# Kernel optimization log

Measured on AMD Instinct MI355X. Metric: run time of the kernel, lower is better.

The kernel has to match this reference:

```python
import jax, jax.numpy as jnp
import numpy as np


def setup_inputs() -> dict:
    key = jax.random.key(0)
    ks = jax.random.split(key, 7)
    b, c, t, h, w = 2, 64, 8, 32, 32
    d = 64
    return {
        "video_features": jax.random.normal(ks[0], (b, c, t, h, w), dtype=jnp.float32),
        "wq": jax.random.normal(ks[1], (d, c), dtype=jnp.float32) * 0.05,
        "bq": jax.random.normal(ks[2], (d,), dtype=jnp.float32) * 0.05,
        "wk": jax.random.normal(ks[3], (d, c), dtype=jnp.float32) * 0.05,
        "bk": jax.random.normal(ks[4], (d,), dtype=jnp.float32) * 0.05,
        "wv": jax.random.normal(ks[5], (d, c), dtype=jnp.float32) * 0.05,
        "bv": jax.random.normal(ks[6], (d,), dtype=jnp.float32) * 0.05,
    }


def reference(video_features, wq, bq, wk, bk, wv, bv):
    b, c, t, h, w = video_features.shape
    d = wq.shape[0]
    xf = video_features.reshape(b, c, t * h * w)  # [b, c, N]
    # 1x1x1 Conv3d == channel-wise linear projection
    q = jnp.einsum('dc,bcn->bnd', wq, xf) + bq                 # [b, N, d]
    k = jnp.einsum('dc,bcn->bnd', wk, xf) + bk                 # [b, N, d]
    v = jnp.einsum('dc,bcn->bnd', wv, xf) + bv                 # [b, N, d]
    scores = jnp.einsum('bnd,bmd->bnm', q, k) / jnp.sqrt(jnp.asarray(d, xf.dtype))  # [b, N, N]
    attn = jax.nn.softmax(scores, axis=-1)
    out = jnp.einsum('bnm,bmd->bnd', attn, v)                  # [b, N, d]
    out = out.transpose(0, 2, 1).reshape(b, d, t, h, w)
    out = out.sum(axis=2).reshape(b, d, 1, h, w)
    return out
```

## Files before the change

kernel.cpp:

```cpp
#include <hip/hip_runtime.h>
#include <math.h>

#define B 2
#define D 64
#define N 8192
#define T 8
#define HW 1024
#define NCH 8
#define KPC (N / NCH)
#define KT 64
#define NT (KPC / KT)
#define QT 256
#define NQT (N / QT)
#define PTS 18

#define LOG2E 1.44269504f

typedef _Float16 half8 __attribute__((ext_vector_type(8)));
typedef _Float16 half4 __attribute__((ext_vector_type(4)));
typedef _Float16 half2 __attribute__((ext_vector_type(2)));
typedef float floatx4 __attribute__((ext_vector_type(4)));

__global__ __launch_bounds__(256)
void proj_kernel(const float* __restrict__ x,
                 const float* __restrict__ wq, const float* __restrict__ bq,
                 const float* __restrict__ wk, const float* __restrict__ bk,
                 const float* __restrict__ wv, const float* __restrict__ bv,
                 _Float16* __restrict__ Qh, _Float16* __restrict__ Kh,
                 _Float16* __restrict__ VTh) {
    int n  = blockIdx.x * 256 + threadIdx.x;
    int d0 = blockIdx.y * 4;
    int b  = blockIdx.z;

    float xcol[64];
    const float* xb = x + (size_t)b * 64 * N + n;
#pragma unroll
    for (int c = 0; c < 64; ++c) xcol[c] = xb[(size_t)c * N];

    float aq[4], ak[4], av[4];
#pragma unroll
    for (int i = 0; i < 4; ++i) { aq[i] = bq[d0+i]; ak[i] = bk[d0+i]; av[i] = bv[d0+i]; }
#pragma unroll
    for (int c = 0; c < 64; ++c) {
        float xv = xcol[c];
#pragma unroll
        for (int i = 0; i < 4; ++i) {
            aq[i] += wq[(d0 + i) * 64 + c] * xv;
            ak[i] += wk[(d0 + i) * 64 + c] * xv;
            av[i] += wv[(d0 + i) * 64 + c] * xv;
        }
    }
    size_t rowb = ((size_t)b * N + n) * 64 + d0;
    half4 hq, hk;
    const float qs = 0.125f * LOG2E;
#pragma unroll
    for (int i = 0; i < 4; ++i) {
        hq[i] = (_Float16)(aq[i] * qs);
        hk[i] = (_Float16)ak[i];
    }
    *(half4*)(Qh + rowb) = hq;
    *(half4*)(Kh + rowb) = hk;
#pragma unroll
    for (int i = 0; i < 4; ++i)
        VTh[((size_t)b * 64 + d0 + i) * N + n] = (_Float16)av[i];
}

__global__ __launch_bounds__(256, 2)
void attn_kernel(const _Float16* __restrict__ Qh, const _Float16* __restrict__ Kh,
                 const _Float16* __restrict__ VTh,
                 _Float16* __restrict__ Opart, float* __restrict__ lpart) {
    __shared__ _Float16 Ks[2][64][72];
    __shared__ _Float16 VTs[2][64][72];

    int bid = blockIdx.x;
    int b   = bid / (NCH * NQT);
    int rem = bid % (NCH * NQT);
    int ch  = rem / NQT;
    int qt  = rem % NQT;
    int q0  = qt * QT;
    int kbase = ch * KPC;

    int tid  = threadIdx.x;
    int wave = tid >> 6;
    int lane = tid & 63;
    int L    = lane & 15;
    int quad = lane >> 4;

    half8 qa[4][2];
#pragma unroll
    for (int g = 0; g < 4; ++g) {
        const _Float16* qrow = Qh + ((size_t)b * N + q0 + wave * 64 + g * 16 + L) * 64;
        qa[g][0] = *(const half8*)(qrow + quad * 8);
        qa[g][1] = *(const half8*)(qrow + 32 + quad * 8);
    }

    floatx4 o[4][4];
    floatx4 lacc[4];
#pragma unroll
    for (int g = 0; g < 4; ++g) {
        lacc[g] = (floatx4)0.f;
#pragma unroll
        for (int s = 0; s < 4; ++s) o[g][s] = (floatx4)0.f;
    }

    half8 ones;
    {
        _Float16 v = (L == 0) ? (_Float16)1.0f : (_Float16)0.0f;
#pragma unroll
        for (int i = 0; i < 8; ++i) ones[i] = v;
    }

    int srow = tid >> 2, sseg = tid & 3;
    const _Float16* Kg = Kh  + (size_t)b * N * 64 + (size_t)sseg * 16;
    const _Float16* Vg = VTh + ((size_t)b * 64 + srow) * N + sseg * 16;

    half8 kr0, kr1, vr0, vr1;
    {
        const _Float16* kp = Kg + (size_t)(kbase + srow) * 64;
        kr0 = *(const half8*)(kp);
        kr1 = *(const half8*)(kp + 8);
        const _Float16* vp = Vg + kbase;
        vr0 = *(const half8*)(vp);
        vr1 = *(const half8*)(vp + 8);
    }
    *(half8*)(&Ks[0][srow][sseg * 16])      = kr0;
    *(half8*)(&Ks[0][srow][sseg * 16 + 8])  = kr1;
    *(half8*)(&VTs[0][srow][sseg * 16])     = vr0;
    *(half8*)(&VTs[0][srow][sseg * 16 + 8]) = vr1;
    __syncthreads();

    for (int kt = 0; kt < NT; ++kt) {
        int cur = kt & 1, nxt = cur ^ 1;
        bool more = (kt + 1 < NT);

        if (more) {
            int kb = kbase + (kt + 1) * KT;
            const _Float16* kp = Kg + (size_t)(kb + srow) * 64;
            kr0 = *(const half8*)(kp);
            kr1 = *(const half8*)(kp + 8);
            const _Float16* vp = Vg + kb;
            vr0 = *(const half8*)(vp);
            vr1 = *(const half8*)(vp + 8);
        }

        half8 kf[4][2], vb[4][2];
#pragma unroll
        for (int sub = 0; sub < 4; ++sub) {
            kf[sub][0] = *(const half8*)(&Ks[cur][sub * 16 + L][quad * 8]);
            kf[sub][1] = *(const half8*)(&Ks[cur][sub * 16 + L][32 + quad * 8]);
            vb[sub][0] = *(const half8*)(&VTs[cur][sub * 16 + L][quad * 8]);
            vb[sub][1] = *(const half8*)(&VTs[cur][sub * 16 + L][32 + quad * 8]);
        }

        _Float16* P0 = &Ks[nxt][wave * 16][0];
        _Float16* P1 = &VTs[nxt][wave * 16][0];

#pragma unroll
        for (int p = 0; p < 2; ++p) {
            floatx4 s[2][4];
#pragma unroll
            for (int sub = 0; sub < 4; ++sub) {
#pragma unroll
                for (int gg = 0; gg < 2; ++gg) {
                    int g = 2 * p + gg;
                    floatx4 acc = (floatx4)0.f;
                    acc = __builtin_amdgcn_mfma_f32_16x16x32_f16(qa[g][0], kf[sub][0], acc, 0, 0, 0);
                    acc = __builtin_amdgcn_mfma_f32_16x16x32_f16(qa[g][1], kf[sub][1], acc, 0, 0, 0);
                    s[gg][sub] = acc;
                }
            }

#pragma unroll
            for (int gg = 0; gg < 2; ++gg)
#pragma unroll
                for (int sub = 0; sub < 4; ++sub)
#pragma unroll
                    for (int r = 0; r < 4; ++r)
                        s[gg][sub][r] = __builtin_amdgcn_exp2f(s[gg][sub][r]);

#pragma unroll
            for (int gg = 0; gg < 2; ++gg) {
                _Float16* Pb = gg ? P1 : P0;
#pragma unroll
                for (int sub = 0; sub < 4; ++sub) {
                    int cb = (sub * 16 + L) * PTS + quad * 4;
                    half2 w0 = {(_Float16)s[gg][sub][0], (_Float16)s[gg][sub][1]};
                    half2 w1 = {(_Float16)s[gg][sub][2], (_Float16)s[gg][sub][3]};
                    *(half2*)(&Pb[cb])     = w0;
                    *(half2*)(&Pb[cb + 2]) = w1;
                }
            }
            half8 pa[2][2];
#pragma unroll
            for (int gg = 0; gg < 2; ++gg) {
                const _Float16* Pb = gg ? P1 : P0;
#pragma unroll
                for (int h = 0; h < 2; ++h) {
                    half8 a;
#pragma unroll
                    for (int j = 0; j < 8; ++j)
                        a[j] = Pb[(h * 32 + quad * 8 + j) * PTS + L];
                    pa[gg][h] = a;
                }
            }

#pragma unroll
            for (int sub = 0; sub < 4; ++sub) {
#pragma unroll
                for (int gg = 0; gg < 2; ++gg) {
                    int g = 2 * p + gg;
                    o[g][sub] = __builtin_amdgcn_mfma_f32_16x16x32_f16(pa[gg][0], vb[sub][0], o[g][sub], 0, 0, 0);
                    o[g][sub] = __builtin_amdgcn_mfma_f32_16x16x32_f16(pa[gg][1], vb[sub][1], o[g][sub], 0, 0, 0);
                }
            }
#pragma unroll
            for (int gg = 0; gg < 2; ++gg) {
                int g = 2 * p + gg;
                lacc[g] = __builtin_amdgcn_mfma_f32_16x16x32_f16(pa[gg][0], ones, lacc[g], 0, 0, 0);
                lacc[g] = __builtin_amdgcn_mfma_f32_16x16x32_f16(pa[gg][1], ones, lacc[g], 0, 0, 0);
            }
        }

        if (more) {
            *(half8*)(&Ks[nxt][srow][sseg * 16])      = kr0;
            *(half8*)(&Ks[nxt][srow][sseg * 16 + 8])  = kr1;
            *(half8*)(&VTs[nxt][srow][sseg * 16])     = vr0;
            *(half8*)(&VTs[nxt][srow][sseg * 16 + 8]) = vr1;
        }
        __syncthreads();
    }

    size_t pb = (size_t)(b * NCH + ch) * N + q0 + wave * 64;
#pragma unroll
    for (int g = 0; g < 4; ++g)
#pragma unroll
        for (int sub = 0; sub < 4; ++sub)
#pragma unroll
            for (int r = 0; r < 4; ++r)
                Opart[(pb + g * 16 + quad * 4 + r) * 64 + sub * 16 + L] =
                    (_Float16)o[g][sub][r];
    if (L == 0) {
#pragma unroll
        for (int g = 0; g < 4; ++g)
#pragma unroll
            for (int r = 0; r < 4; ++r)
                lpart[pb + g * 16 + quad * 4 + r] = lacc[g][r];
    }
}

__global__ void reduce_kernel(const _Float16* __restrict__ Opart,
                              const float* __restrict__ lpart,
                              float* __restrict__ out) {
    int g  = blockIdx.x * 256 + threadIdx.x;
    int d  = g & 63;
    int hw = (g >> 6) & (HW - 1);
    int b  = g >> 16;

    float acc = 0.f;
    for (int t = 0; t < T; ++t) {
        int row = t * HW + hw;
        float Lsum = 0.f, num = 0.f;
#pragma unroll
        for (int c = 0; c < NCH; ++c) {
            size_t pb = (size_t)(b * NCH + c) * N + row;
            Lsum += lpart[pb];
            num  += (float)Opart[pb * 64 + d];
        }
        acc += num / Lsum;
    }
    out[((size_t)b * D + d) * HW + hw] = acc;
}

extern "C" void kernel_launch(void* const* d_in, const int* in_sizes, int n_in,
                              void* d_out, int out_size, void* d_ws, size_t ws_size,
                              hipStream_t stream) {
    const float* x  = (const float*)d_in[0];
    const float* wq = (const float*)d_in[1];
    const float* bq = (const float*)d_in[2];
    const float* wk = (const float*)d_in[3];
    const float* bk = (const float*)d_in[4];
    const float* wv = (const float*)d_in[5];
    const float* bv = (const float*)d_in[6];

    const size_t QSZ = (size_t)B * N * 64;
    _Float16* Qh    = (_Float16*)d_ws;
    _Float16* Kh    = Qh + QSZ;
    _Float16* VTh   = Kh + QSZ;
    _Float16* Opart = VTh + QSZ;
    float*    lpart = (float*)(Opart + (size_t)B * NCH * N * 64);

    proj_kernel<<<dim3(N / 256, 16, B), 256, 0, stream>>>(x, wq, bq, wk, bk, wv, bv,
                                                          Qh, Kh, VTh);
    attn_kernel<<<B * NCH * NQT, 256, 0, stream>>>(Qh, Kh, VTh, Opart, lpart);
    reduce_kernel<<<(B * HW * D) / 256, 256, 0, stream>>>(Opart, lpart, (float*)d_out);
}
```

Measured before the change: 138.0 us.

## Stage input tile in shared memory and compute eight output channels per thread

The projection kernel now loads a 64x32 tile of input columns into shared memory once per block, and each thread computes 8 output dims instead of 4 for one position. This removes the 16x redundant global reads of x across the old grid's d-dimension, and the Q/K stores widen to 8-half vectors. Weight loads per thread double, the block count drops to 512, and each half-wavefront in a warp reads different weight rows.

```diff
diff --git a/kernel.cpp b/kernel.cpp
--- a/kernel.cpp
+++ b/kernel.cpp
@@ -28,40 +28,52 @@
                  const float* __restrict__ wv, const float* __restrict__ bv,
                  _Float16* __restrict__ Qh, _Float16* __restrict__ Kh,
                  _Float16* __restrict__ VTh) {
-    int n  = blockIdx.x * 256 + threadIdx.x;
-    int d0 = blockIdx.y * 4;
-    int b  = blockIdx.z;
-
-    float xcol[64];
-    const float* xb = x + (size_t)b * 64 * N + n;
-#pragma unroll
-    for (int c = 0; c < 64; ++c) xcol[c] = xb[(size_t)c * N];
-
-    float aq[4], ak[4], av[4];
-#pragma unroll
-    for (int i = 0; i < 4; ++i) { aq[i] = bq[d0+i]; ak[i] = bk[d0+i]; av[i] = bv[d0+i]; }
+    __shared__ float xs[64][32];
+
+    int bid = blockIdx.x;
+    int b   = bid / (N / 32);
+    int n0  = (bid % (N / 32)) * 32;
+
+    int tid  = threadIdx.x;
+    int nl   = tid & 31;
+    int dg   = tid >> 5;
+    int d0   = dg * 8;
+
+    {
+        int cs = tid >> 5;
+        const float* xb = x + (size_t)b * 64 * N + n0 + nl;
+#pragma unroll
+        for (int k = 0; k < 8; ++k)
+            xs[cs + 8 * k][nl] = xb[(size_t)(cs + 8 * k) * N];
+    }
+    __syncthreads();
+
+    float aq[8], ak[8], av[8];
+#pragma unroll
+    for (int i = 0; i < 8; ++i) { aq[i] = bq[d0+i]; ak[i] = bk[d0+i]; av[i] = bv[d0+i]; }
 #pragma unroll
     for (int c = 0; c < 64; ++c) {
-        float xv = xcol[c];
-#pragma unroll
-        for (int i = 0; i < 4; ++i) {
+        float xv = xs[c][nl];
+#pragma unroll
+        for (int i = 0; i < 8; ++i) {
             aq[i] += wq[(d0 + i) * 64 + c] * xv;
             ak[i] += wk[(d0 + i) * 64 + c] * xv;
             av[i] += wv[(d0 + i) * 64 + c] * xv;
         }
     }
+    int n = n0 + nl;
     size_t rowb = ((size_t)b * N + n) * 64 + d0;
-    half4 hq, hk;
+    half8 hq, hk;
     const float qs = 0.125f * LOG2E;
 #pragma unroll
-    for (int i = 0; i < 4; ++i) {
+    for (int i = 0; i < 8; ++i) {
         hq[i] = (_Float16)(aq[i] * qs);
         hk[i] = (_Float16)ak[i];
     }
-    *(half4*)(Qh + rowb) = hq;
-    *(half4*)(Kh + rowb) = hk;
-#pragma unroll
-    for (int i = 0; i < 4; ++i)
+    *(half8*)(Qh + rowb) = hq;
+    *(half8*)(Kh + rowb) = hk;
+#pragma unroll
+    for (int i = 0; i < 8; ++i)
         VTh[((size_t)b * 64 + d0 + i) * N + n] = (_Float16)av[i];
 }
 
@@ -289,8 +301,8 @@
     _Float16* Opart = VTh + QSZ;
     float*    lpart = (float*)(Opart + (size_t)B * NCH * N * 64);
 
-    proj_kernel<<<dim3(N / 256, 16, B), 256, 0, stream>>>(x, wq, bq, wk, bk, wv, bv,
-                                                          Qh, Kh, VTh);
+    proj_kernel<<<B * (N / 32), 256, 0, stream>>>(x, wq, bq, wk, bk, wv, bv,
+                                                  Qh, Kh, VTh);
     attn_kernel<<<B * NCH * NQT, 256, 0, stream>>>(Qh, Kh, VTh, Opart, lpart);
     reduce_kernel<<<(B * HW * D) / 256, 256, 0, stream>>>(Opart, lpart, (float*)d_out);
 }
```

After: 148.3 us. +7.4%, slower.
